# Optimization experiments

Measured on AMD Instinct MI355X. Metric: run time of the kernel, lower is better.

The kernel has to match this reference:

```python
import jax, jax.numpy as jnp
import numpy as np

NUM_HEADS = 8
NUM_LEVELS = 4
NUM_POINTS = 8
EMBED = 256
SPATIAL_SHAPES = ((92, 160), (46, 80), (23, 40), (12, 20))


def _bilinear_sample(vl, gx, gy, H, W):
    # vl: [N, d, H*W]; gx, gy: [N, Q, P], grid coords in [-1, 1]
    # matches F.grid_sample(mode='bilinear', padding_mode='zeros', align_corners=False)
    x = (gx + 1.0) * (W * 0.5) - 0.5
    y = (gy + 1.0) * (H * 0.5) - 0.5
    x0 = jnp.floor(x)
    y0 = jnp.floor(y)
    wx = x - x0
    wy = y - y0
    x0i = x0.astype(jnp.int32)
    y0i = y0.astype(jnp.int32)
    N, Q, P = gx.shape
    d = vl.shape[1]

    def gather(xi, yi):
        valid = ((xi >= 0) & (xi < W) & (yi >= 0) & (yi < H)).astype(vl.dtype)
        idx = jnp.clip(yi, 0, H - 1) * W + jnp.clip(xi, 0, W - 1)  # [N, Q, P]
        flat = jnp.broadcast_to(idx.reshape(N, 1, Q * P), (N, d, Q * P))
        got = jnp.take_along_axis(vl, flat, axis=2).reshape(N, d, Q, P)
        return got * valid[:, None]

    return (gather(x0i, y0i) * ((1 - wx) * (1 - wy))[:, None]
            + gather(x0i + 1, y0i) * (wx * (1 - wy))[:, None]
            + gather(x0i, y0i + 1) * ((1 - wx) * wy)[:, None]
            + gather(x0i + 1, y0i + 1) * (wx * wy)[:, None])


def _forward(query, value, reference_points, spatial_shapes,
             W_off, b_off, W_attn, b_attn, W_val, b_val, W_out, b_out):
    shapes = np.asarray(spatial_shapes)  # static per-level (H, W)
    bs, Q, C = query.shape
    H, Lv, P = NUM_HEADS, NUM_LEVELS, NUM_POINTS
    d = C // H
    # value projection, split into heads: [bs*H, d, Ltot]
    v = value @ W_val + b_val
    v = v.reshape(bs, -1, H, d).transpose(0, 2, 3, 1).reshape(bs * H, d, -1)
    # sampling offsets [bs, Q, H, Lv, P, 2]
    off = (query @ W_off + b_off).reshape(bs, Q, H, Lv, P, 2)
    # attention weights, softmax over Lv*P
    aw = jax.nn.softmax((query @ W_attn + b_attn).reshape(bs, Q, H, Lv * P), axis=-1)
    aw = aw.reshape(bs, Q, H, Lv, P).transpose(0, 2, 1, 3, 4).reshape(bs * H, Q, Lv, P)
    # normalize offsets by level (W, H)
    norm = jnp.asarray([[w_, h_] for h_, w_ in shapes], dtype=query.dtype)  # [Lv, 2]
    loc = reference_points[:, :, None, :, None, :] + off / norm[None, None, None, :, None, :]
    grids = (2.0 * loc - 1.0).transpose(0, 2, 1, 3, 4, 5).reshape(bs * H, Q, Lv, P, 2)
    out = jnp.zeros((bs * H, d, Q), dtype=query.dtype)
    start = 0
    for lvl in range(Lv):
        H_l, W_l = int(shapes[lvl, 0]), int(shapes[lvl, 1])
        vl = v[:, :, start:start + H_l * W_l]
        g = grids[:, :, lvl]  # [bs*H, Q, P, 2]
        s = _bilinear_sample(vl, g[..., 0], g[..., 1], H_l, W_l)  # [bs*H, d, Q, P]
        out = out + jnp.einsum('ndqp,nqp->ndq', s, aw[:, :, lvl])
        start += H_l * W_l
    out = out.reshape(bs, H, d, Q).transpose(0, 3, 1, 2).reshape(bs, Q, C)
    return out @ W_out + b_out


def setup_inputs() -> dict:
    key = jax.random.key(0)
    ks = jax.random.split(key, 9)
    bs, Q = 6, 4096  # 6 cameras x (64x64 BEV queries)
    Ltot = sum(h * w for h, w in SPATIAL_SHAPES)  # 19560
    HLP2 = NUM_HEADS * NUM_LEVELS * NUM_POINTS * 2  # 512
    HLP = NUM_HEADS * NUM_LEVELS * NUM_POINTS  # 256
    s = 0.02
    return {
        "query": jax.random.normal(ks[0], (bs, Q, EMBED), jnp.float32),
        "value": jax.random.normal(ks[1], (bs, Ltot, EMBED), jnp.float32),
        "reference_points": jax.random.uniform(ks[2], (bs, Q, NUM_LEVELS, 2), jnp.float32),
        "spatial_shapes": jnp.asarray(SPATIAL_SHAPES, jnp.int32),
        "W_off": s * jax.random.normal(ks[3], (EMBED, HLP2), jnp.float32),
        "b_off": s * jax.random.normal(ks[4], (HLP2,), jnp.float32),
        "W_attn": s * jax.random.normal(ks[5], (EMBED, HLP), jnp.float32),
        "b_attn": s * jax.random.normal(ks[6], (HLP,), jnp.float32),
        "W_val": s * jax.random.normal(ks[7], (EMBED, EMBED), jnp.float32),
        "b_val": jnp.zeros((EMBED,), jnp.float32),
        "W_out": s * jax.random.normal(ks[8], (EMBED, EMBED), jnp.float32),
        "b_out": jnp.zeros((EMBED,), jnp.float32),
    }


def reference(query, value, reference_points, spatial_shapes,
              W_off, b_off, W_attn, b_attn, W_val, b_val, W_out, b_out):
    return _forward(query, value, reference_points, spatial_shapes,
                    W_off, b_off, W_attn, b_attn, W_val, b_val, W_out, b_out)
```

## Files before the change

kernel.cpp:

```cpp
#include <hip/hip_runtime.h>
#include <stdint.h>

#define BS 6
#define NQ 4096
#define NH 8
#define EMB 256
#define LTOT 19560
#define ROWS_V 117360
#define ROWS_VP 117376
#define ROWS_Q 24576

typedef __attribute__((ext_vector_type(8))) short bf16x8;
typedef __attribute__((ext_vector_type(4))) float floatx4;

__device__ __forceinline__ ushort f2bf(float f) {
    union { float f; uint32_t i; } c; c.f = f;
    uint32_t r = c.i + 0x7FFFu + ((c.i >> 16) & 1u);
    return (ushort)(r >> 16);
}
__device__ __forceinline__ float bflo(uint32_t u) {
    union { uint32_t i; float f; } c; c.i = u << 16; return c.f;
}
__device__ __forceinline__ float bfhi(uint32_t u) {
    union { uint32_t i; float f; } c; c.i = u & 0xFFFF0000u; return c.f;
}

__device__ __forceinline__ void gll16(const ushort* g, ushort* l) {
    __builtin_amdgcn_global_load_lds(
        (const __attribute__((address_space(1))) void*)g,
        (__attribute__((address_space(3))) void*)l, 16, 0, 0);
}

#define FMA4(d, s, v) \
    (d).x = fmaf((s), (v).x, (d).x); \
    (d).y = fmaf((s), (v).y, (d).y); \
    (d).z = fmaf((s), (v).z, (d).z); \
    (d).w = fmaf((s), (v).w, (d).w);

__global__ __launch_bounds__(256) void cast_bf16(
    const float* __restrict__ in, ushort* __restrict__ out, int n, int n_pad)
{
    int i = (blockIdx.x * 256 + threadIdx.x) * 8;
    if (i >= n_pad) return;
    ushort4 r0, r1;
    if (i < n) {
        float4 f0 = *(const float4*)(in + i);
        float4 f1 = *(const float4*)(in + i + 4);
        r0.x = f2bf(f0.x); r0.y = f2bf(f0.y); r0.z = f2bf(f0.z); r0.w = f2bf(f0.w);
        r1.x = f2bf(f1.x); r1.y = f2bf(f1.y); r1.z = f2bf(f1.z); r1.w = f2bf(f1.w);
    } else {
        r0.x = r0.y = r0.z = r0.w = 0;
        r1 = r0;
    }
    *(ushort4*)(out + i) = r0;
    *(ushort4*)(out + i + 4) = r1;
}

__global__ __launch_bounds__(256) void cast_t(
    const float* __restrict__ W, ushort* __restrict__ Wt, int N_)
{
    int id = blockIdx.x * 256 + threadIdx.x;
    if (id >= 256 * N_) return;
    int n = id >> 8;
    int k = id & 255;
    Wt[id] = f2bf(W[(size_t)k * N_ + n]);
}

template<bool OUT_BF16>
__global__ __launch_bounds__(256) void gemm_bt(
    const ushort* __restrict__ A,
    const ushort* __restrict__ Bt,
    const float* __restrict__ bias,
    void* __restrict__ Cv, int M, int N)
{
    constexpr int K = 256;
    __shared__ ushort As[128 * 32];
    __shared__ ushort Bs[128 * 32];

    const int t = threadIdx.x;
    const int w = t >> 6;
    const int lane = t & 63;
    const int bm = blockIdx.x * 128;
    const int bn = blockIdx.y * 128;
    const int wm = (w >> 1) * 64;
    const int wn = (w & 1) * 64;

    floatx4 acc[4][4] = {};

    const int srow = lane >> 2;
    const int scol = (lane & 3) * 8;
    const ushort* Ag0 = A + (size_t)(bm + (w * 2 + 0) * 16 + srow) * K + scol;
    const ushort* Ag1 = A + (size_t)(bm + (w * 2 + 1) * 16 + srow) * K + scol;
    const ushort* Bg0 = Bt + (size_t)(bn + (w * 2 + 0) * 16 + srow) * K + scol;
    const ushort* Bg1 = Bt + (size_t)(bn + (w * 2 + 1) * 16 + srow) * K + scol;
    ushort* Al0 = &As[(w * 2 + 0) * 512];
    ushort* Al1 = &As[(w * 2 + 1) * 512];
    ushort* Bl0 = &Bs[(w * 2 + 0) * 512];
    ushort* Bl1 = &Bs[(w * 2 + 1) * 512];

    const ushort* apt = &As[(wm + (lane & 15)) * 32 + (lane >> 4) * 8];
    const ushort* bpt = &Bs[(wn + (lane & 15)) * 32 + (lane >> 4) * 8];

    for (int kt = 0; kt < K; kt += 32) {
        __syncthreads();
        gll16(Ag0 + kt, Al0);
        gll16(Ag1 + kt, Al1);
        gll16(Bg0 + kt, Bl0);
        gll16(Bg1 + kt, Bl1);
        __syncthreads();

        bf16x8 a[4], b[4];
        #pragma unroll
        for (int i = 0; i < 4; ++i) {
            a[i] = *(const bf16x8*)(apt + i * 16 * 32);
            b[i] = *(const bf16x8*)(bpt + i * 16 * 32);
        }
        #pragma unroll
        for (int i = 0; i < 4; ++i)
            #pragma unroll
            for (int j = 0; j < 4; ++j)
                acc[i][j] = __builtin_amdgcn_mfma_f32_16x16x32_bf16(
                    a[i], b[j], acc[i][j], 0, 0, 0);
    }

    const int crow = (lane >> 4) * 4;
    const int ccol = lane & 15;
    #pragma unroll
    for (int j = 0; j < 4; ++j) {
        int gcol = bn + wn + j * 16 + ccol;
        float bv = bias[gcol];
        #pragma unroll
        for (int i = 0; i < 4; ++i) {
            #pragma unroll
            for (int r = 0; r < 4; ++r) {
                int grow = bm + wm + i * 16 + crow + r;
                if (grow < M) {
                    float val = acc[i][j][r] + bv;
                    if (OUT_BF16)
                        ((ushort*)Cv)[(size_t)grow * N + gcol] = f2bf(val);
                    else
                        ((float*)Cv)[(size_t)grow * N + gcol] = val;
                }
            }
        }
    }
}

__global__ __launch_bounds__(256) void gemm128(
    const float* __restrict__ A, const float* __restrict__ B,
    const float* __restrict__ bias, float* __restrict__ C,
    int M, int N)
{
    constexpr int K = 256;
    __shared__ float Asm[8][128];
    __shared__ float Bsm[8][128];

    const int t  = threadIdx.x;
    const int bm = blockIdx.x * 128;
    const int bn = blockIdx.y * 128;
    const int tx = t & 15;
    const int ty = t >> 4;

    const int arow = t >> 1;
    const int akv  = (t & 1) * 4;
    const int brow = t >> 5;
    const int bcol = (t & 31) * 4;

    const bool arowok = (bm + arow) < M;
    const float* Aptr = A + (size_t)(bm + arow) * K + akv;
    const float* Bptr = B + (size_t)brow * N + bn + bcol;

    float4 acc[2][2][4];
    #pragma unroll
    for (int i = 0; i < 2; ++i)
        #pragma unroll
        for (int j = 0; j < 2; ++j)
            #pragma unroll
            for (int e = 0; e < 4; ++e)
                acc[i][j][e] = make_float4(0.f, 0.f, 0.f, 0.f);

    for (int kt = 0; kt < K; kt += 8) {
        float4 af = arowok ? *(const float4*)(Aptr + kt)
                           : make_float4(0.f, 0.f, 0.f, 0.f);
        float4 bf = *(const float4*)(Bptr + (size_t)kt * N);

        __syncthreads();
        Asm[akv + 0][arow] = af.x;
        Asm[akv + 1][arow] = af.y;
        Asm[akv + 2][arow] = af.z;
        Asm[akv + 3][arow] = af.w;
        *(float4*)&Bsm[brow][bcol] = bf;
        __syncthreads();

        #pragma unroll
        for (int k = 0; k < 8; ++k) {
            float4 a0 = *(const float4*)&Asm[k][ty * 4];
            float4 a1 = *(const float4*)&Asm[k][ty * 4 + 64];
            float4 b0 = *(const float4*)&Bsm[k][tx * 4];
            float4 b1 = *(const float4*)&Bsm[k][tx * 4 + 64];
            float ar[8] = {a0.x, a0.y, a0.z, a0.w, a1.x, a1.y, a1.z, a1.w};
            #pragma unroll
            for (int i = 0; i < 2; ++i) {
                #pragma unroll
                for (int e = 0; e < 4; ++e) {
                    float a = ar[i * 4 + e];
                    FMA4(acc[i][0][e], a, b0);
                    FMA4(acc[i][1][e], a, b1);
                }
            }
        }
    }

    float4 bias0 = *(const float4*)(bias + bn + tx * 4);
    float4 bias1 = *(const float4*)(bias + bn + 64 + tx * 4);

    #pragma unroll
    for (int i = 0; i < 2; ++i) {
        #pragma unroll
        for (int e = 0; e < 4; ++e) {
            int row = bm + i * 64 + ty * 4 + e;
            if (row < M) {
                float4 r0 = acc[i][0][e];
                r0.x += bias0.x; r0.y += bias0.y; r0.z += bias0.z; r0.w += bias0.w;
                *(float4*)(C + (size_t)row * N + bn + tx * 4) = r0;
                float4 r1 = acc[i][1][e];
                r1.x += bias1.x; r1.y += bias1.y; r1.z += bias1.z; r1.w += bias1.w;
                *(float4*)(C + (size_t)row * N + bn + 64 + tx * 4) = r1;
            }
        }
    }
}

__global__ __launch_bounds__(256) void softmax32(
    const float* __restrict__ in, float* __restrict__ out, int rows)
{
    int r = blockIdx.x * blockDim.x + threadIdx.x;
    if (r >= rows) return;
    const float* p = in + (size_t)r * 32;
    float v[32];
    #pragma unroll
    for (int i = 0; i < 8; ++i)
        *(float4*)&v[i * 4] = *(const float4*)(p + i * 4);
    float m = v[0];
    #pragma unroll
    for (int i = 1; i < 32; ++i) m = fmaxf(m, v[i]);
    float s = 0.f;
    #pragma unroll
    for (int i = 0; i < 32; ++i) { v[i] = __expf(v[i] - m); s += v[i]; }
    float inv = 1.f / s;
    float* q = out + (size_t)r * 32;
    #pragma unroll
    for (int i = 0; i < 8; ++i) {
        float4 wv = make_float4(v[i*4] * inv, v[i*4+1] * inv, v[i*4+2] * inv, v[i*4+3] * inv);
        *(float4*)(q + i * 4) = wv;
    }
}

__global__ __launch_bounds__(256) void sampler4(
    const ushort* __restrict__ v,
    const float* __restrict__ off,
    const float* __restrict__ aw,
    const float* __restrict__ ref,
    float* __restrict__ agg)
{
    const int tid = threadIdx.x;
    const int g = blockIdx.x * 64 + (tid >> 2);
    const int st = tid & 3;
    const int h = g & 7;
    const int bq = g >> 3;
    const int b = bq >> 12;

    float o[16];
    {
        const float* offp = off + (size_t)bq * 512 + h * 64 + st * 16;
        #pragma unroll
        for (int i = 0; i < 4; ++i)
            *(float4*)&o[i * 4] = *(const float4*)(offp + i * 4);
    }
    float a8[8];
    {
        const float* awp = aw + (size_t)bq * 256 + h * 32 + st * 8;
        *(float4*)&a8[0] = *(const float4*)(awp);
        *(float4*)&a8[4] = *(const float4*)(awp + 4);
    }
    float rf[8];
    *(float4*)&rf[0] = *(const float4*)(ref + (size_t)bq * 8);
    *(float4*)&rf[4] = *(const float4*)(ref + (size_t)bq * 8 + 4);

    const ushort* vb = v + (size_t)b * LTOT * EMB + h * 32 + st * 8;

    const int LW[4] = {160, 80, 40, 20};
    const int LH[4] = {92, 46, 23, 12};
    const int LS[4] = {0, 14720, 18400, 19320};

    float acc[8] = {0.f, 0.f, 0.f, 0.f, 0.f, 0.f, 0.f, 0.f};

    #pragma unroll
    for (int k = 0; k < 32; ++k) {
        const int l = k >> 3;
        const int W = LW[l], Hh = LH[l], S = LS[l];
        const int src = k >> 3;
        const int idx = k & 7;
        float awk = __shfl(a8[idx], k >> 3, 4);
        float ox  = __shfl(o[2 * idx], k >> 3, 4);
        float oy  = __shfl(o[2 * idx + 1], k >> 3, 4);
        (void)src;

        float px = fmaf(rf[2 * l], (float)W, ox) - 0.5f;
        float py = fmaf(rf[2 * l + 1], (float)Hh, oy) - 0.5f;
        float x0f = floorf(px), y0f = floorf(py);
        float wx = px - x0f, wy = py - y0f;
        int x0 = (int)x0f, y0 = (int)y0f;
        int x1 = x0 + 1, y1 = y0 + 1;

        float vx0 = (x0 >= 0 && x0 < W) ? 1.f : 0.f;
        float vx1 = (x1 >= 0 && x1 < W) ? 1.f : 0.f;
        float vy0 = (y0 >= 0 && y0 < Hh) ? 1.f : 0.f;
        float vy1 = (y1 >= 0 && y1 < Hh) ? 1.f : 0.f;
        int cx0 = min(max(x0, 0), W - 1);
        int cx1 = min(max(x1, 0), W - 1);
        int cy0 = min(max(y0, 0), Hh - 1);
        int cy1 = min(max(y1, 0), Hh - 1);

        float w00 = (1.f - wx) * (1.f - wy) * vx0 * vy0 * awk;
        float w10 = wx * (1.f - wy) * vx1 * vy0 * awk;
        float w01 = (1.f - wx) * wy * vx0 * vy1 * awk;
        float w11 = wx * wy * vx1 * vy1 * awk;

        uint4 c00 = *(const uint4*)(vb + (size_t)(S + cy0 * W + cx0) * EMB);
        uint4 c10 = *(const uint4*)(vb + (size_t)(S + cy0 * W + cx1) * EMB);
        uint4 c01 = *(const uint4*)(vb + (size_t)(S + cy1 * W + cx0) * EMB);
        uint4 c11 = *(const uint4*)(vb + (size_t)(S + cy1 * W + cx1) * EMB);

        #define ACC8(w_, c_) \
            acc[0] = fmaf(w_, bflo(c_.x), acc[0]); acc[1] = fmaf(w_, bfhi(c_.x), acc[1]); \
            acc[2] = fmaf(w_, bflo(c_.y), acc[2]); acc[3] = fmaf(w_, bfhi(c_.y), acc[3]); \
            acc[4] = fmaf(w_, bflo(c_.z), acc[4]); acc[5] = fmaf(w_, bfhi(c_.z), acc[5]); \
            acc[6] = fmaf(w_, bflo(c_.w), acc[6]); acc[7] = fmaf(w_, bfhi(c_.w), acc[7]);
        ACC8(w00, c00);
        ACC8(w10, c10);
        ACC8(w01, c01);
        ACC8(w11, c11);
        #undef ACC8
    }

    float* ap = agg + (size_t)bq * 256 + h * 32 + st * 8;
    *(float4*)ap       = make_float4(acc[0], acc[1], acc[2], acc[3]);
    *(float4*)(ap + 4) = make_float4(acc[4], acc[5], acc[6], acc[7]);
}

extern "C" void kernel_launch(void* const* d_in, const int* in_sizes, int n_in,
                              void* d_out, int out_size, void* d_ws, size_t ws_size,
                              hipStream_t stream) {
    const float* query  = (const float*)d_in[0];
    const float* value  = (const float*)d_in[1];
    const float* refpts = (const float*)d_in[2];
    const float* W_off  = (const float*)d_in[4];
    const float* b_off  = (const float*)d_in[5];
    const float* W_attn = (const float*)d_in[6];
    const float* b_attn = (const float*)d_in[7];
    const float* W_val  = (const float*)d_in[8];
    const float* b_val  = (const float*)d_in[9];
    const float* W_out  = (const float*)d_in[10];
    const float* b_out  = (const float*)d_in[11];
    float* out = (float*)d_out;

    char* ws = (char*)d_ws;
    ushort* v_bf   = (ushort*)(ws);
    ushort* val_bf = (ushort*)(ws + 60096512ull);
    float*  agg    = (float*) (ws + 60096512ull);
    ushort* q_bf   = (ushort*)(ws + 120193024ull);
    float*  off_b  = (float*) (ws + 132775936ull);
    float*  attn_b = (float*) (ws + 183107584ull);
    ushort* Wvt    = (ushort*)(ws + 208273408ull);
    ushort* Woft   = (ushort*)(ws + 208404480ull);
    ushort* Wat    = (ushort*)(ws + 208666624ull);

    cast_bf16<<<(ROWS_VP * EMB / 8) / 256, 256, 0, stream>>>(
        value, val_bf, ROWS_V * EMB, ROWS_VP * EMB);
    cast_bf16<<<(ROWS_Q * EMB / 8) / 256, 256, 0, stream>>>(
        query, q_bf, ROWS_Q * EMB, ROWS_Q * EMB);
    cast_t<<<(256 * 256) / 256, 256, 0, stream>>>(W_val, Wvt, 256);
    cast_t<<<(256 * 512) / 256, 256, 0, stream>>>(W_off, Woft, 512);
    cast_t<<<(256 * 256) / 256, 256, 0, stream>>>(W_attn, Wat, 256);

    gemm_bt<true><<<dim3(ROWS_VP / 128, 2), 256, 0, stream>>>(
        val_bf, Wvt, b_val, v_bf, ROWS_V, 256);

    gemm_bt<false><<<dim3(ROWS_Q / 128, 4), 256, 0, stream>>>(
        q_bf, Woft, b_off, off_b, ROWS_Q, 512);
    gemm_bt<false><<<dim3(ROWS_Q / 128, 2), 256, 0, stream>>>(
        q_bf, Wat, b_attn, attn_b, ROWS_Q, 256);

    softmax32<<<(ROWS_Q * NH) / 256, 256, 0, stream>>>(
        attn_b, attn_b, ROWS_Q * NH);

    sampler4<<<(ROWS_Q * NH) / 64, 256, 0, stream>>>(
        v_bf, off_b, attn_b, refpts, agg);

    gemm128<<<dim3(ROWS_Q / 128, 2), 256, 0, stream>>>(
        agg, W_out, b_out, out, ROWS_Q, 256);
}
```

Before: 483.0 us.

## Fuse value cast into GEMM, merge query projections, fold softmax into sampler

The value projection now reads fp32 directly and converts to bf16 while staging into LDS, so the separate cast pass and its intermediate buffer go away. The offset and attention projections are merged into a single 768-wide GEMM with a concatenated bias. Softmax is computed inside the sampler using 4-lane shuffles, which removes a separate kernel and a round trip through memory. The sampler writes bf16 output, so the final output projection can run on the MFMA bf16 GEMM in place of the scalar fp32 GEMM, at the cost of extra rounding error.

```diff
diff --git a/kernel.cpp b/kernel.cpp
--- a/kernel.cpp
+++ b/kernel.cpp
@@ -12,6 +12,7 @@
 
 typedef __attribute__((ext_vector_type(8))) short bf16x8;
 typedef __attribute__((ext_vector_type(4))) float floatx4;
+typedef __attribute__((ext_vector_type(8))) unsigned short ushort8v;
 
 __device__ __forceinline__ ushort f2bf(float f) {
     union { float f; uint32_t i; } c; c.f = f;
@@ -31,29 +32,17 @@
         (__attribute__((address_space(3))) void*)l, 16, 0, 0);
 }
 
-#define FMA4(d, s, v) \
-    (d).x = fmaf((s), (v).x, (d).x); \
-    (d).y = fmaf((s), (v).y, (d).y); \
-    (d).z = fmaf((s), (v).z, (d).z); \
-    (d).w = fmaf((s), (v).w, (d).w);
-
 __global__ __launch_bounds__(256) void cast_bf16(
-    const float* __restrict__ in, ushort* __restrict__ out, int n, int n_pad)
+    const float* __restrict__ in, ushort* __restrict__ out, int n)
 {
     int i = (blockIdx.x * 256 + threadIdx.x) * 8;
-    if (i >= n_pad) return;
-    ushort4 r0, r1;
-    if (i < n) {
-        float4 f0 = *(const float4*)(in + i);
-        float4 f1 = *(const float4*)(in + i + 4);
-        r0.x = f2bf(f0.x); r0.y = f2bf(f0.y); r0.z = f2bf(f0.z); r0.w = f2bf(f0.w);
-        r1.x = f2bf(f1.x); r1.y = f2bf(f1.y); r1.z = f2bf(f1.z); r1.w = f2bf(f1.w);
-    } else {
-        r0.x = r0.y = r0.z = r0.w = 0;
-        r1 = r0;
-    }
-    *(ushort4*)(out + i) = r0;
-    *(ushort4*)(out + i + 4) = r1;
+    if (i >= n) return;
+    float4 f0 = *(const float4*)(in + i);
+    float4 f1 = *(const float4*)(in + i + 4);
+    ushort8v r;
+    r[0] = f2bf(f0.x); r[1] = f2bf(f0.y); r[2] = f2bf(f0.z); r[3] = f2bf(f0.w);
+    r[4] = f2bf(f1.x); r[5] = f2bf(f1.y); r[6] = f2bf(f1.z); r[7] = f2bf(f1.w);
+    *(ushort8v*)(out + i) = r;
 }
 
 __global__ __launch_bounds__(256) void cast_t(
@@ -66,12 +55,104 @@
     Wt[id] = f2bf(W[(size_t)k * N_ + n]);
 }
 
-template<bool OUT_BF16>
+__global__ __launch_bounds__(768) void bias_concat(
+    const float* __restrict__ b_off, const float* __restrict__ b_attn,
+    float* __restrict__ bcat)
+{
+    int i = threadIdx.x;
+    bcat[i] = (i < 512) ? b_off[i] : b_attn[i - 512];
+}
+
+__global__ __launch_bounds__(512) void vgemm(
+    const float* __restrict__ A,
+    const ushort* __restrict__ Bt,
+    const float* __restrict__ bias,
+    ushort* __restrict__ C)
+{
+    constexpr int K = 256, N = 256, M = ROWS_V;
+    __shared__ ushort As[128 * 32];
+    __shared__ ushort Bs[256 * 32];
+
+    const int t = threadIdx.x;
+    const int w = t >> 6;
+    const int lane = t & 63;
+    const int bm = blockIdx.x * 128;
+    const int wm = (w >> 2) * 64;
+    const int wn = (w & 3) * 64;
+
+    const int arow = t >> 2;
+    const int acol = (t & 3) * 8;
+    const bool rowok = (bm + arow) < M;
+    const float* Ap = A + (size_t)(bm + arow) * K + acol;
+    ushort* Asw = &As[arow * 32 + acol];
+
+    const int srow = lane >> 2;
+    const int scol = (lane & 3) * 8;
+    const ushort* Bg0 = Bt + (size_t)(w * 32 + srow) * K + scol;
+    const ushort* Bg1 = Bt + (size_t)(w * 32 + 16 + srow) * K + scol;
+    ushort* Bl0 = &Bs[(w * 32) * 32];
+    ushort* Bl1 = &Bs[(w * 32 + 16) * 32];
+
+    const ushort* apt = &As[(wm + (lane & 15)) * 32 + (lane >> 4) * 8];
+    const ushort* bpt = &Bs[(wn + (lane & 15)) * 32 + (lane >> 4) * 8];
+
+    floatx4 acc[4][4] = {};
+
+    for (int kt = 0; kt < K; kt += 32) {
+        float4 f0, f1;
+        if (rowok) {
+            f0 = *(const float4*)(Ap + kt);
+            f1 = *(const float4*)(Ap + kt + 4);
+        } else {
+            f0 = make_float4(0.f, 0.f, 0.f, 0.f);
+            f1 = f0;
+        }
+        __syncthreads();
+        gll16(Bg0 + kt, Bl0);
+        gll16(Bg1 + kt, Bl1);
+        ushort8v u;
+        u[0] = f2bf(f0.x); u[1] = f2bf(f0.y); u[2] = f2bf(f0.z); u[3] = f2bf(f0.w);
+        u[4] = f2bf(f1.x); u[5] = f2bf(f1.y); u[6] = f2bf(f1.z); u[7] = f2bf(f1.w);
+        *(ushort8v*)Asw = u;
+        __syncthreads();
+
+        bf16x8 a[4], b[4];
+        #pragma unroll
+        for (int i = 0; i < 4; ++i) {
+            a[i] = *(const bf16x8*)(apt + i * 16 * 32);
+            b[i] = *(const bf16x8*)(bpt + i * 16 * 32);
+        }
+        #pragma unroll
+        for (int i = 0; i < 4; ++i)
+            #pragma unroll
+            for (int j = 0; j < 4; ++j)
+                acc[i][j] = __builtin_amdgcn_mfma_f32_16x16x32_bf16(
+                    a[i], b[j], acc[i][j], 0, 0, 0);
+    }
+
+    const int crow = (lane >> 4) * 4;
+    const int ccol = lane & 15;
+    #pragma unroll
+    for (int j = 0; j < 4; ++j) {
+        int gcol = wn + j * 16 + ccol;
+        float bv = bias[gcol];
+        #pragma unroll
+        for (int i = 0; i < 4; ++i) {
+            #pragma unroll
+            for (int r = 0; r < 4; ++r) {
+                int grow = bm + wm + i * 16 + crow + r;
+                if (grow < M)
+                    C[(size_t)grow * N + gcol] = f2bf(acc[i][j][r] + bv);
+            }
+        }
+    }
+}
+
 __global__ __launch_bounds__(256) void gemm_bt(
     const ushort* __restrict__ A,
     const ushort* __restrict__ Bt,
     const float* __restrict__ bias,
-    void* __restrict__ Cv, int M, int N)
+    float* __restrict__ C, int M, int N)
 {
     constexpr int K = 256;
     __shared__ ushort As[128 * 32];
@@ -134,134 +215,18 @@
             #pragma unroll
             for (int r = 0; r < 4; ++r) {
                 int grow = bm + wm + i * 16 + crow + r;
-                if (grow < M) {
-                    float val = acc[i][j][r] + bv;
-                    if (OUT_BF16)
-                        ((ushort*)Cv)[(size_t)grow * N + gcol] = f2bf(val);
-                    else
-                        ((float*)Cv)[(size_t)grow * N + gcol] = val;
-                }
+                if (grow < M)
+                    C[(size_t)grow * N + gcol] = acc[i][j][r] + bv;
             }
         }
-    }
-}
-
-__global__ __launch_bounds__(256) void gemm128(
-    const float* __restrict__ A, const float* __restrict__ B,
-    const float* __restrict__ bias, float* __restrict__ C,
-    int M, int N)
-{
-    constexpr int K = 256;
-    __shared__ float Asm[8][128];
-    __shared__ float Bsm[8][128];
-
-    const int t  = threadIdx.x;
-    const int bm = blockIdx.x * 128;
-    const int bn = blockIdx.y * 128;
-    const int tx = t & 15;
-    const int ty = t >> 4;
-
-    const int arow = t >> 1;
-    const int akv  = (t & 1) * 4;
-    const int brow = t >> 5;
-    const int bcol = (t & 31) * 4;
-
-    const bool arowok = (bm + arow) < M;
-    const float* Aptr = A + (size_t)(bm + arow) * K + akv;
-    const float* Bptr = B + (size_t)brow * N + bn + bcol;
-
-    float4 acc[2][2][4];
-    #pragma unroll
-    for (int i = 0; i < 2; ++i)
-        #pragma unroll
-        for (int j = 0; j < 2; ++j)
-            #pragma unroll
-            for (int e = 0; e < 4; ++e)
-                acc[i][j][e] = make_float4(0.f, 0.f, 0.f, 0.f);
-
-    for (int kt = 0; kt < K; kt += 8) {
-        float4 af = arowok ? *(const float4*)(Aptr + kt)
-                           : make_float4(0.f, 0.f, 0.f, 0.f);
-        float4 bf = *(const float4*)(Bptr + (size_t)kt * N);
-
-        __syncthreads();
-        Asm[akv + 0][arow] = af.x;
-        Asm[akv + 1][arow] = af.y;
-        Asm[akv + 2][arow] = af.z;
-        Asm[akv + 3][arow] = af.w;
-        *(float4*)&Bsm[brow][bcol] = bf;
-        __syncthreads();
-
-        #pragma unroll
-        for (int k = 0; k < 8; ++k) {
-            float4 a0 = *(const float4*)&Asm[k][ty * 4];
-            float4 a1 = *(const float4*)&Asm[k][ty * 4 + 64];
-            float4 b0 = *(const float4*)&Bsm[k][tx * 4];
-            float4 b1 = *(const float4*)&Bsm[k][tx * 4 + 64];
-            float ar[8] = {a0.x, a0.y, a0.z, a0.w, a1.x, a1.y, a1.z, a1.w};
-            #pragma unroll
-            for (int i = 0; i < 2; ++i) {
-                #pragma unroll
-                for (int e = 0; e < 4; ++e) {
-                    float a = ar[i * 4 + e];
-                    FMA4(acc[i][0][e], a, b0);
-                    FMA4(acc[i][1][e], a, b1);
-                }
-            }
-        }
-    }
-
-    float4 bias0 = *(const float4*)(bias + bn + tx * 4);
-    float4 bias1 = *(const float4*)(bias + bn + 64 + tx * 4);
-
-    #pragma unroll
-    for (int i = 0; i < 2; ++i) {
-        #pragma unroll
-        for (int e = 0; e < 4; ++e) {
-            int row = bm + i * 64 + ty * 4 + e;
-            if (row < M) {
-                float4 r0 = acc[i][0][e];
-                r0.x += bias0.x; r0.y += bias0.y; r0.z += bias0.z; r0.w += bias0.w;
-                *(float4*)(C + (size_t)row * N + bn + tx * 4) = r0;
-                float4 r1 = acc[i][1][e];
-                r1.x += bias1.x; r1.y += bias1.y; r1.z += bias1.z; r1.w += bias1.w;
-                *(float4*)(C + (size_t)row * N + bn + 64 + tx * 4) = r1;
-            }
-        }
-    }
-}
-
-__global__ __launch_bounds__(256) void softmax32(
-    const float* __restrict__ in, float* __restrict__ out, int rows)
-{
-    int r = blockIdx.x * blockDim.x + threadIdx.x;
-    if (r >= rows) return;
-    const float* p = in + (size_t)r * 32;
-    float v[32];
-    #pragma unroll
-    for (int i = 0; i < 8; ++i)
-        *(float4*)&v[i * 4] = *(const float4*)(p + i * 4);
-    float m = v[0];
-    #pragma unroll
-    for (int i = 1; i < 32; ++i) m = fmaxf(m, v[i]);
-    float s = 0.f;
-    #pragma unroll
-    for (int i = 0; i < 32; ++i) { v[i] = __expf(v[i] - m); s += v[i]; }
-    float inv = 1.f / s;
-    float* q = out + (size_t)r * 32;
-    #pragma unroll
-    for (int i = 0; i < 8; ++i) {
-        float4 wv = make_float4(v[i*4] * inv, v[i*4+1] * inv, v[i*4+2] * inv, v[i*4+3] * inv);
-        *(float4*)(q + i * 4) = wv;
     }
 }
 
 __global__ __launch_bounds__(256) void sampler4(
     const ushort* __restrict__ v,
-    const float* __restrict__ off,
-    const float* __restrict__ aw,
+    const float* __restrict__ qp,
     const float* __restrict__ ref,
-    float* __restrict__ agg)
+    ushort* __restrict__ agg)
 {
     const int tid = threadIdx.x;
     const int g = blockIdx.x * 64 + (tid >> 2);
@@ -272,16 +237,29 @@
 
     float o[16];
     {
-        const float* offp = off + (size_t)bq * 512 + h * 64 + st * 16;
+        const float* offp = qp + (size_t)bq * 768 + h * 64 + st * 16;
         #pragma unroll
         for (int i = 0; i < 4; ++i)
             *(float4*)&o[i * 4] = *(const float4*)(offp + i * 4);
     }
     float a8[8];
     {
-        const float* awp = aw + (size_t)bq * 256 + h * 32 + st * 8;
-        *(float4*)&a8[0] = *(const float4*)(awp);
-        *(float4*)&a8[4] = *(const float4*)(awp + 4);
+        const float* lp = qp + (size_t)bq * 768 + 512 + h * 32 + st * 8;
+        *(float4*)&a8[0] = *(const float4*)(lp);
+        *(float4*)&a8[4] = *(const float4*)(lp + 4);
+        float m = a8[0];
+        #pragma unroll
+        for (int i = 1; i < 8; ++i) m = fmaxf(m, a8[i]);
+        m = fmaxf(m, __shfl_xor(m, 1, 4));
+        m = fmaxf(m, __shfl_xor(m, 2, 4));
+        float s = 0.f;
+        #pragma unroll
+        for (int i = 0; i < 8; ++i) { a8[i] = __expf(a8[i] - m); s += a8[i]; }
+        s += __shfl_xor(s, 1, 4);
+        s += __shfl_xor(s, 2, 4);
+        float inv = 1.f / s;
+        #pragma unroll
+        for (int i = 0; i < 8; ++i) a8[i] *= inv;
     }
     float rf[8];
     *(float4*)&rf[0] = *(const float4*)(ref + (size_t)bq * 8);
@@ -299,12 +277,10 @@
     for (int k = 0; k < 32; ++k) {
         const int l = k >> 3;
         const int W = LW[l], Hh = LH[l], S = LS[l];
-        const int src = k >> 3;
         const int idx = k & 7;
         float awk = __shfl(a8[idx], k >> 3, 4);
         float ox  = __shfl(o[2 * idx], k >> 3, 4);
         float oy  = __shfl(o[2 * idx + 1], k >> 3, 4);
-        (void)src;
 
         float px = fmaf(rf[2 * l], (float)W, ox) - 0.5f;
         float py = fmaf(rf[2 * l + 1], (float)Hh, oy) - 0.5f;
@@ -344,9 +320,10 @@
         #undef ACC8
     }
 
-    float* ap = agg + (size_t)bq * 256 + h * 32 + st * 8;
-    *(float4*)ap       = make_float4(acc[0], acc[1], acc[2], acc[3]);
-    *(float4*)(ap + 4) = make_float4(acc[4], acc[5], acc[6], acc[7]);
+    ushort8v r;
+    #pragma unroll
+    for (int i = 0; i < 8; ++i) r[i] = f2bf(acc[i]);
+    *(ushort8v*)(agg + (size_t)bq * 256 + h * 32 + st * 8) = r;
 }
 
 extern "C" void kernel_launch(void* const* d_in, const int* in_sizes, int n_in,
@@ -367,37 +344,30 @@
 
     char* ws = (char*)d_ws;
     ushort* v_bf   = (ushort*)(ws);
-    ushort* val_bf = (ushort*)(ws + 60096512ull);
-    float*  agg    = (float*) (ws + 60096512ull);
-    ushort* q_bf   = (ushort*)(ws + 120193024ull);
-    float*  off_b  = (float*) (ws + 132775936ull);
-    float*  attn_b = (float*) (ws + 183107584ull);
-    ushort* Wvt    = (ushort*)(ws + 208273408ull);
-    ushort* Woft   = (ushort*)(ws + 208404480ull);
-    ushort* Wat    = (ushort*)(ws + 208666624ull);
-
-    cast_bf16<<<(ROWS_VP * EMB / 8) / 256, 256, 0, stream>>>(
-        value, val_bf, ROWS_V * EMB, ROWS_VP * EMB);
+    ushort* q_bf   = (ushort*)(ws + 60096512ull);
+    float*  qp     = (float*) (ws + 72679424ull);
+    ushort* agg_bf = (ushort*)(ws + 148176896ull);
+    ushort* Wvt    = (ushort*)(ws + 160759808ull);
+    ushort* Wq     = (ushort*)(ws + 160890880ull);
+    ushort* Wot    = (ushort*)(ws + 161284096ull);
+    float*  bcat   = (float*) (ws + 161415168ull);
+
+    cast_t<<<(256 * 256) / 256, 256, 0, stream>>>(W_val, Wvt, 256);
+    cast_t<<<(256 * 512) / 256, 256, 0, stream>>>(W_off, Wq, 512);
+    cast_t<<<(256 * 256) / 256, 256, 0, stream>>>(W_attn, Wq + 512 * 256, 256);
+    cast_t<<<(256 * 256) / 256, 256, 0, stream>>>(W_out, Wot, 256);
+    bias_concat<<<1, 768, 0, stream>>>(b_off, b_attn, bcat);
     cast_bf16<<<(ROWS_Q * EMB / 8) / 256, 256, 0, stream>>>(
-        query, q_bf, ROWS_Q * EMB, ROWS_Q * EMB);
-    cast_t<<<(256 * 256) / 256, 256, 0, stream>>>(W_val, Wvt, 256);
-    cast_t<<<(256 * 512) / 256, 256, 0, stream>>>(W_off, Woft, 512);
-    cast_t<<<(256 * 256) / 256, 256, 0, stream>>>(W_attn, Wat, 256);
-
-    gemm_bt<true><<<dim3(ROWS_VP / 128, 2), 256, 0, stream>>>(
-        val_bf, Wvt, b_val, v_bf, ROWS_V, 256);
-
-    gemm_bt<false><<<dim3(ROWS_Q / 128, 4), 256, 0, stream>>>(
-        q_bf, Woft, b_off, off_b, ROWS_Q, 512);
-    gemm_bt<false><<<dim3(ROWS_Q / 128, 2), 256, 0, stream>>>(
-        q_bf, Wat, b_attn, attn_b, ROWS_Q, 256);
-
-    softmax32<<<(ROWS_Q * NH) / 256, 256, 0, stream>>>(
-        attn_b, attn_b, ROWS_Q * NH);
+        query, q_bf, ROWS_Q * EMB);
+
+    vgemm<<<ROWS_VP / 128, 512, 0, stream>>>(value, Wvt, b_val, v_bf);
+
+    gemm_bt<<<dim3(ROWS_Q / 128, 6), 256, 0, stream>>>(
+        q_bf, Wq, bcat, qp, ROWS_Q, 768);
 
     sampler4<<<(ROWS_Q * NH) / 64, 256, 0, stream>>>(
-        v_bf, off_b, attn_b, refpts, agg);
-
-    gemm128<<<dim3(ROWS_Q / 128, 2), 256, 0, stream>>>(
-        agg, W_out, b_out, out, ROWS_Q, 256);
-}
+        v_bf, qp, refpts, agg_bf);
+
+    gemm_bt<<<dim3(ROWS_Q / 128, 2), 256, 0, stream>>>(
+        agg_bf, Wot, b_out, out, ROWS_Q, 256);
+}
```

Measured after the change: 416.4 us. 1.16x faster.
